# Performance work log

Hardware: AMD Instinct MI355X
Metric: run time of the kernel (lower is better)

Reference implementation:

```python
import jax, jax.numpy as jnp
import numpy as np

TEMPERATURE = 0.5
EPS = 1e-12  # torch F.normalize eps


def setup_inputs() -> dict:
    key = jax.random.key(0)
    k1, k2 = jax.random.split(key)
    z_i = jax.random.normal(k1, (32, 128, 128), dtype=jnp.float32)
    z_j = jax.random.normal(k2, (32, 128, 128), dtype=jnp.float32)
    return {"z_i": z_i, "z_j": z_j}


def _l2_normalize(x):
    # matches torch F.normalize(dim=1): x / max(||x||, eps)
    n = jnp.sqrt(jnp.sum(x * x, axis=1, keepdims=True))
    return x / jnp.maximum(n, EPS)


def _off_diagonal(a):
    # rows of a with the diagonal removed, row-major order -> [n, n-1]
    n = a.shape[0]
    return a.reshape(-1)[:-1].reshape(n - 1, n + 1)[:, 1:].reshape(n, n - 1)


def reference(z_i, z_j):
    B, S, D = z_i.shape
    N = B * S
    zi = _l2_normalize(z_i.reshape(N, D))
    zj = _l2_normalize(z_j.reshape(N, D))
    r = jnp.concatenate([zi, zj], axis=0)              # [2N, D]
    sim = r @ r.T                                      # [2N, 2N]
    # positives: off-diagonals at +/-N (unaffected by the diag -inf fill)
    pos = jnp.concatenate([jnp.diagonal(sim, N), jnp.diagonal(sim, -N)])  # [2N]
    # negatives: all non-diagonal entries, row-major (== torch boolean-mask view)
    neg = _off_diagonal(sim)                           # [2N, 2N-1]
    logits = jnp.concatenate([pos[:, None], neg], axis=1) / TEMPERATURE  # [2N, 2N]
    # labels are all 0 -> CE(sum) / 2N == mean of -log_softmax[:, 0]
    loss = -jax.nn.log_softmax(logits, axis=1)[:, 0]
    return jnp.sum(loss) / (2 * N)
```

## Files before the change

kernel.cpp:

```cpp
#include <hip/hip_runtime.h>
#include <hip/hip_bf16.h>
#include <math.h>

#define NPAIR 4096
#define D 128
#define TWO_N 8192
#define NSLAB 32
#define ALPHA 1.6986436f

typedef float f32x4 __attribute__((ext_vector_type(4)));
typedef long lx2 __attribute__((ext_vector_type(2)));

__device__ __forceinline__ void async_ld16(void* lds, const void* g) {
    __builtin_amdgcn_global_load_lds(
        (__attribute__((address_space(1))) const unsigned int*)g,
        (__attribute__((address_space(3))) unsigned int*)lds, 16, 0, 0);
}

__global__ __launch_bounds__(256) void norm_kernel(const float* __restrict__ zi,
                                                   const float* __restrict__ zj,
                                                   unsigned char* __restrict__ Rb,
                                                   float* __restrict__ pos,
                                                   float* __restrict__ out) {
    if (blockIdx.x == 0 && threadIdx.x == 0) out[0] = 0.f;
    int k = blockIdx.x * 4 + (threadIdx.x >> 6);
    int t = threadIdx.x & 63;
    const float2 a = *(const float2*)(zi + k * D + 2 * t);
    const float2 b = *(const float2*)(zj + k * D + 2 * t);
    float si = a.x * a.x + a.y * a.y;
    float sj = b.x * b.x + b.y * b.y;
    float dt = a.x * b.x + a.y * b.y;
    #pragma unroll
    for (int m = 1; m < 64; m <<= 1) {
        si += __shfl_xor(si, m, 64);
        sj += __shfl_xor(sj, m, 64);
        dt += __shfl_xor(dt, m, 64);
    }
    float ii = 1.0f / fmaxf(sqrtf(si), 1e-12f);
    float ij = 1.0f / fmaxf(sqrtf(sj), 1e-12f);
    if (t == 0) pos[k] = dt * ii * ij;
    ii *= ALPHA; ij *= ALPHA;
    int c = t >> 2;
    int posb = (c & 3) * 32 + (c >> 2) * 8 + 2 * (t & 3);
    int r0 = __builtin_amdgcn_cvt_pk_fp8_f32(a.x * ii, a.y * ii, 0, false);
    *(unsigned short*)(Rb + (size_t)k * 128 + posb) = (unsigned short)r0;
    int r1 = __builtin_amdgcn_cvt_pk_fp8_f32(b.x * ij, b.y * ij, 0, false);
    *(unsigned short*)(Rb + (size_t)(k + NPAIR) * 128 + posb) = (unsigned short)r1;
}

__global__ __launch_bounds__(256, 4) void simexp_kernel(const unsigned char* __restrict__ Rb,
                                                        float* __restrict__ rspart) {
    __shared__ uint4 Bs[4][3][128];
    const int bi = blockIdx.x >> 3;
    const int jc = blockIdx.x & 7;
    const int tid = threadIdx.x;
    const int wave = tid >> 6, lane = tid & 63;
    const int rp = lane & 15, q = lane >> 4;

    long afr[4][4];
    {
        const unsigned char* Ab = Rb + (size_t)(bi * 64 + rp) * 128 + q * 32;
        #pragma unroll
        for (int rt = 0; rt < 4; ++rt) {
            lx2 h0 = *(const lx2*)(Ab + rt * 16 * 128);
            lx2 h1 = *(const lx2*)(Ab + rt * 16 * 128 + 16);
            afr[0][rt] = h0.x;  afr[1][rt] = h0.y;
            afr[2][rt] = h1.x;  afr[3][rt] = h1.y;
        }
    }

    const unsigned char* gslab = Rb + (size_t)(jc * 1024 + wave * 16) * 128;
    char* lpanel = (char*)&Bs[wave][0][0];
    const int laneoff = (lane >> 3) * 128 + (((lane & 7) ^ ((lane >> 3) & 7)) << 4);

    float rs[16];
    #pragma unroll
    for (int i = 0; i < 16; ++i) rs[i] = 0.f;

    #pragma unroll
    for (int j = 0; j < 2; ++j)
        #pragma unroll
        for (int d = 0; d < 2; ++d)
            async_ld16(lpanel + j * 2048 + d * 1024,
                       gslab + j * 8192 + d * 1024 + laneoff);

    const int diagbase = bi * 64 - jc * 1024;
    const int slot0 = rp * 8;
    const int sw = rp & 7;

    #pragma unroll
    for (int jt = 0; jt < 16; ++jt) {
        if (jt < 14) __builtin_amdgcn_s_waitcnt(0x0F72);
        else         __builtin_amdgcn_s_waitcnt(0x0F70);

        const int cur = jt % 3;
        const uint4* P = &Bs[wave][cur][0];
        lx2 v0 = *(const lx2*)&P[slot0 + ((q * 2 + 0) ^ sw)];
        lx2 v1 = *(const lx2*)&P[slot0 + ((q * 2 + 1) ^ sw)];

        if (jt < 14) {
            const int nb = (jt + 2) % 3;
            #pragma unroll
            for (int d = 0; d < 2; ++d)
                async_ld16(lpanel + nb * 2048 + d * 1024,
                           gslab + (jt + 2) * 8192 + d * 1024 + laneoff);
        }

        f32x4 acc[4] = {};
        #pragma unroll
        for (int rt = 0; rt < 4; ++rt) {
            acc[rt] = __builtin_amdgcn_mfma_f32_16x16x32_fp8_fp8(afr[0][rt], v0.x, acc[rt], 0, 0, 0);
            acc[rt] = __builtin_amdgcn_mfma_f32_16x16x32_fp8_fp8(afr[1][rt], v0.y, acc[rt], 0, 0, 0);
            acc[rt] = __builtin_amdgcn_mfma_f32_16x16x32_fp8_fp8(afr[2][rt], v1.x, acc[rt], 0, 0, 0);
            acc[rt] = __builtin_amdgcn_mfma_f32_16x16x32_fp8_fp8(afr[3][rt], v1.y, acc[rt], 0, 0, 0);
        }

        if (jt * 64 == diagbase) {
            #pragma unroll
            for (int rt = 0; rt < 4; ++rt)
                #pragma unroll
                for (int r = 0; r < 4; ++r) {
                    int ro = rt * 16 + q * 4 + r;
                    int co = wave * 16 + rp;
                    float e = __builtin_amdgcn_exp2f(acc[rt][r]);
                    rs[rt * 4 + r] += (ro == co) ? 0.f : e;
                }
        } else {
            #pragma unroll
            for (int rt = 0; rt < 4; ++rt)
                #pragma unroll
                for (int r = 0; r < 4; ++r)
                    rs[rt * 4 + r] += __builtin_amdgcn_exp2f(acc[rt][r]);
        }
    }

    #pragma unroll
    for (int i = 0; i < 16; ++i) {
        float v = rs[i];
        v += __shfl_xor(v, 1, 64);
        v += __shfl_xor(v, 2, 64);
        v += __shfl_xor(v, 4, 64);
        v += __shfl_xor(v, 8, 64);
        rs[i] = v;
    }
    if (rp == 0) {
        const int slab = jc * 4 + wave;
        const int rowb = bi * 64 + q * 4;
        #pragma unroll
        for (int rt = 0; rt < 4; ++rt)
            #pragma unroll
            for (int r = 0; r < 4; ++r)
                rspart[slab * TWO_N + rowb + rt * 16 + r] = rs[rt * 4 + r];
    }
}

__global__ __launch_bounds__(256) void finalize_kernel(const float* __restrict__ rspart,
                                                       const float* __restrict__ pos,
                                                       float* __restrict__ out) {
    __shared__ float red[4];
    int tid = threadIdx.x;
    float local = 0.f;
    #pragma unroll
    for (int i = 0; i < 2; ++i) {
        int k = blockIdx.x * 512 + i * 256 + tid;
        float rsum = 0.f;
        #pragma unroll
        for (int p = 0; p < NSLAB; ++p) rsum += rspart[p * TWO_N + k];
        float ps = pos[k & (NPAIR - 1)];
        float p2 = ps + ps;
        local += logf(rsum + __expf(p2)) - p2;
    }
    #pragma unroll
    for (int m = 1; m < 64; m <<= 1) local += __shfl_xor(local, m, 64);
    if ((tid & 63) == 0) red[tid >> 6] = local;
    __syncthreads();
    if (tid == 0) {
        float s = red[0] + red[1] + red[2] + red[3];
        atomicAdd(out, s * (1.0f / (float)TWO_N));
    }
}

extern "C" void kernel_launch(void* const* d_in, const int* in_sizes, int n_in,
                              void* d_out, int out_size, void* d_ws, size_t ws_size,
                              hipStream_t stream) {
    const float* zi = (const float*)d_in[0];
    const float* zj = (const float*)d_in[1];
    char* ws = (char*)d_ws;
    unsigned char* Rb = (unsigned char*)ws;
    float* rspart = (float*)(ws + 1 * 1024 * 1024);
    float* pos = (float*)(ws + 2 * 1024 * 1024);

    norm_kernel<<<NPAIR / 4, 256, 0, stream>>>(zi, zj, Rb, pos, (float*)d_out);
    simexp_kernel<<<128 * 8, 256, 0, stream>>>(Rb, rspart);
    finalize_kernel<<<16, 256, 0, stream>>>(rspart, pos, (float*)d_out);
}
```

Before: 78.96 us.

## Exploit similarity symmetry: compute upper-triangle tiles with row and column sums

```diff
diff --git a/kernel.cpp b/kernel.cpp
--- a/kernel.cpp
+++ b/kernel.cpp
@@ -5,7 +5,6 @@
 #define NPAIR 4096
 #define D 128
 #define TWO_N 8192
-#define NSLAB 32
 #define ALPHA 1.6986436f
 
 typedef float f32x4 __attribute__((ext_vector_type(4)));
@@ -21,8 +20,10 @@
                                                    const float* __restrict__ zj,
                                                    unsigned char* __restrict__ Rb,
                                                    float* __restrict__ pos,
+                                                   float* __restrict__ rowsum,
                                                    float* __restrict__ out) {
-    if (blockIdx.x == 0 && threadIdx.x == 0) out[0] = 0.f;
+    if (threadIdx.x < 8) rowsum[blockIdx.x * 8 + threadIdx.x] = 0.f;
+    if (blockIdx.x == 0 && threadIdx.x == 8) out[0] = 0.f;
     int k = blockIdx.x * 4 + (threadIdx.x >> 6);
     int t = threadIdx.x & 63;
     const float2 a = *(const float2*)(zi + k * D + 2 * t);
@@ -49,17 +50,23 @@
 }
 
 __global__ __launch_bounds__(256, 4) void simexp_kernel(const unsigned char* __restrict__ Rb,
-                                                        float* __restrict__ rspart) {
+                                                        float* __restrict__ rowsum) {
     __shared__ uint4 Bs[4][3][128];
-    const int bi = blockIdx.x >> 3;
-    const int jc = blockIdx.x & 7;
+    const int pair = blockIdx.x >> 4;
+    const int jc = blockIdx.x & 15;
+    const int biA = pair, biB = 127 - pair;
+    const int nA = 128 - biA;
+    const int start = (jc * 129) >> 4;
+    const int end = ((jc + 1) * 129) >> 4;
+    const int n = end - start;
+
     const int tid = threadIdx.x;
     const int wave = tid >> 6, lane = tid & 63;
     const int rp = lane & 15, q = lane >> 4;
 
     long afr[4][4];
-    {
-        const unsigned char* Ab = Rb + (size_t)(bi * 64 + rp) * 128 + q * 32;
+    auto loadA = [&](int s) {
+        const unsigned char* Ab = Rb + (size_t)(s * 64 + rp) * 128 + q * 32;
         #pragma unroll
         for (int rt = 0; rt < 4; ++rt) {
             lx2 h0 = *(const lx2*)(Ab + rt * 16 * 128);
@@ -67,44 +74,57 @@
             afr[0][rt] = h0.x;  afr[1][rt] = h0.y;
             afr[2][rt] = h1.x;  afr[3][rt] = h1.y;
         }
-    }
-
-    const unsigned char* gslab = Rb + (size_t)(jc * 1024 + wave * 16) * 128;
+    };
+    auto coltile = [&](int idx) { return (idx < nA) ? (biA + idx) : (idx - 1); };
+
     char* lpanel = (char*)&Bs[wave][0][0];
     const int laneoff = (lane >> 3) * 128 + (((lane & 7) ^ ((lane >> 3) & 7)) << 4);
+    auto prefetch_tile = [&](int ct, int buf) {
+        const unsigned char* g = Rb + (size_t)(ct * 64 + wave * 16) * 128 + laneoff;
+        async_ld16(lpanel + buf * 2048, g);
+        async_ld16(lpanel + buf * 2048 + 1024, g + 1024);
+    };
 
     float rs[16];
     #pragma unroll
     for (int i = 0; i < 16; ++i) rs[i] = 0.f;
-
-    #pragma unroll
-    for (int j = 0; j < 2; ++j)
+    auto flush_rows = [&](int s) {
         #pragma unroll
-        for (int d = 0; d < 2; ++d)
-            async_ld16(lpanel + j * 2048 + d * 1024,
-                       gslab + j * 8192 + d * 1024 + laneoff);
-
-    const int diagbase = bi * 64 - jc * 1024;
-    const int slot0 = rp * 8;
-    const int sw = rp & 7;
-
-    #pragma unroll
-    for (int jt = 0; jt < 16; ++jt) {
-        if (jt < 14) __builtin_amdgcn_s_waitcnt(0x0F72);
-        else         __builtin_amdgcn_s_waitcnt(0x0F70);
-
-        const int cur = jt % 3;
-        const uint4* P = &Bs[wave][cur][0];
+        for (int i = 0; i < 16; ++i) {
+            float v = rs[i];
+            v += __shfl_xor(v, 1, 64);
+            v += __shfl_xor(v, 2, 64);
+            v += __shfl_xor(v, 4, 64);
+            v += __shfl_xor(v, 8, 64);
+            if (rp == 0)
+                atomicAdd(&rowsum[s * 64 + (i >> 2) * 16 + q * 4 + (i & 3)], v);
+            rs[i] = 0.f;
+        }
+    };
+
+    loadA(start < nA ? biA : biB);
+    prefetch_tile(coltile(start), 0);
+    prefetch_tile(coltile(start + 1), 1);
+
+    float csum[9];
+    const int slot0 = rp * 8, sw = rp & 7;
+
+    #pragma unroll
+    for (int i = 0; i < 9; ++i) {
+        if (i >= n) break;
+        const int idx = start + i;
+        if (i > 0 && idx == nA) {
+            flush_rows(biA);
+            loadA(biB);
+        }
+        if (i + 1 < n) __builtin_amdgcn_s_waitcnt(0x0F72);
+        else           __builtin_amdgcn_s_waitcnt(0x0F70);
+
+        const uint4* P = &Bs[wave][i % 3][0];
         lx2 v0 = *(const lx2*)&P[slot0 + ((q * 2 + 0) ^ sw)];
         lx2 v1 = *(const lx2*)&P[slot0 + ((q * 2 + 1) ^ sw)];
 
-        if (jt < 14) {
-            const int nb = (jt + 2) % 3;
-            #pragma unroll
-            for (int d = 0; d < 2; ++d)
-                async_ld16(lpanel + nb * 2048 + d * 1024,
-                           gslab + (jt + 2) * 8192 + d * 1024 + laneoff);
-        }
+        if (i + 2 < n) prefetch_tile(coltile(idx + 2), (i + 2) % 3);
 
         f32x4 acc[4] = {};
         #pragma unroll
@@ -115,7 +135,8 @@
             acc[rt] = __builtin_amdgcn_mfma_f32_16x16x32_fp8_fp8(afr[3][rt], v1.y, acc[rt], 0, 0, 0);
         }
 
-        if (jt * 64 == diagbase) {
+        float cs = 0.f;
+        if (idx == 0 || idx == nA) {
             #pragma unroll
             for (int rt = 0; rt < 4; ++rt)
                 #pragma unroll
@@ -129,32 +150,31 @@
             #pragma unroll
             for (int rt = 0; rt < 4; ++rt)
                 #pragma unroll
-                for (int r = 0; r < 4; ++r)
-                    rs[rt * 4 + r] += __builtin_amdgcn_exp2f(acc[rt][r]);
-        }
-    }
-
-    #pragma unroll
-    for (int i = 0; i < 16; ++i) {
-        float v = rs[i];
-        v += __shfl_xor(v, 1, 64);
-        v += __shfl_xor(v, 2, 64);
-        v += __shfl_xor(v, 4, 64);
-        v += __shfl_xor(v, 8, 64);
-        rs[i] = v;
-    }
-    if (rp == 0) {
-        const int slab = jc * 4 + wave;
-        const int rowb = bi * 64 + q * 4;
-        #pragma unroll
-        for (int rt = 0; rt < 4; ++rt)
-            #pragma unroll
-            for (int r = 0; r < 4; ++r)
-                rspart[slab * TWO_N + rowb + rt * 16 + r] = rs[rt * 4 + r];
-    }
-}
-
-__global__ __launch_bounds__(256) void finalize_kernel(const float* __restrict__ rspart,
+                for (int r = 0; r < 4; ++r) {
+                    float e = __builtin_amdgcn_exp2f(acc[rt][r]);
+                    rs[rt * 4 + r] += e;
+                    cs += e;
+                }
+        }
+        csum[i] = cs;
+    }
+
+    flush_rows((end - 1 < nA) ? biA : biB);
+
+    #pragma unroll
+    for (int i = 0; i < 9; ++i) {
+        if (i >= n) break;
+        const int idx = start + i;
+        if (idx == 0 || idx == nA) continue;
+        float v = csum[i];
+        v += __shfl_xor(v, 16, 64);
+        v += __shfl_xor(v, 32, 64);
+        if (q == 0)
+            atomicAdd(&rowsum[coltile(idx) * 64 + wave * 16 + rp], v);
+    }
+}
+
+__global__ __launch_bounds__(256) void finalize_kernel(const float* __restrict__ rowsum,
                                                        const float* __restrict__ pos,
                                                        float* __restrict__ out) {
     __shared__ float red[4];
@@ -163,12 +183,9 @@
     #pragma unroll
     for (int i = 0; i < 2; ++i) {
         int k = blockIdx.x * 512 + i * 256 + tid;
-        float rsum = 0.f;
-        #pragma unroll
-        for (int p = 0; p < NSLAB; ++p) rsum += rspart[p * TWO_N + k];
         float ps = pos[k & (NPAIR - 1)];
         float p2 = ps + ps;
-        local += logf(rsum + __expf(p2)) - p2;
+        local += logf(rowsum[k] + __expf(p2)) - p2;
     }
     #pragma unroll
     for (int m = 1; m < 64; m <<= 1) local += __shfl_xor(local, m, 64);
@@ -187,10 +204,10 @@
     const float* zj = (const float*)d_in[1];
     char* ws = (char*)d_ws;
     unsigned char* Rb = (unsigned char*)ws;
-    float* rspart = (float*)(ws + 1 * 1024 * 1024);
-    float* pos = (float*)(ws + 2 * 1024 * 1024);
-
-    norm_kernel<<<NPAIR / 4, 256, 0, stream>>>(zi, zj, Rb, pos, (float*)d_out);
-    simexp_kernel<<<128 * 8, 256, 0, stream>>>(Rb, rspart);
-    finalize_kernel<<<16, 256, 0, stream>>>(rspart, pos, (float*)d_out);
-}
+    float* rowsum = (float*)(ws + 1024 * 1024);
+    float* pos = (float*)(ws + 1024 * 1024 + 32 * 1024);
+
+    norm_kernel<<<NPAIR / 4, 256, 0, stream>>>(zi, zj, Rb, pos, rowsum, (float*)d_out);
+    simexp_kernel<<<64 * 16, 256, 0, stream>>>(Rb, rowsum);
+    finalize_kernel<<<16, 256, 0, stream>>>(rowsum, pos, (float*)d_out);
+}
```

After: 84.22 us. 1.07x slower.
